# Kernel tuning notes

Measured on AMD Instinct MI355X. Metric: run time of the kernel, lower is better.

Reference implementation:

```python
import jax, jax.numpy as jnp
import numpy as np

M = 8      # number of modalities (len(ModalityType))
D = 256    # embedding_dim
B = 8192   # batch size


def setup_inputs() -> dict:
    key = jax.random.key(0)
    ks = jax.random.split(key, 12)
    s = 1.0 / np.sqrt(D)
    x = jax.random.normal(ks[0], (M, B, D), dtype=jnp.float32)
    reasoning_query = jax.random.normal(ks[1], (B, D), dtype=jnp.float32)
    # Per ordered modality pair (src, tgt): seq_len=1 MHA reduces to out_proj(V_proj(tgt)).
    Wv = jax.random.normal(ks[2], (M, M, D, D), dtype=jnp.float32) * s
    bv = jnp.zeros((M, M, D), dtype=jnp.float32)
    Wo = jax.random.normal(ks[3], (M, M, D, D), dtype=jnp.float32) * s
    bo = jnp.zeros((M, M, D), dtype=jnp.float32)
    # Per-modality fusion MLP: Linear(2D->D), ReLU, Linear(D->D)  (dropout = eval/identity)
    W1 = jax.random.normal(ks[4], (M, D, 2 * D), dtype=jnp.float32) * s
    b1 = jnp.zeros((M, D), dtype=jnp.float32)
    W2 = jax.random.normal(ks[5], (M, D, D), dtype=jnp.float32) * s
    b2 = jnp.zeros((M, D), dtype=jnp.float32)
    # Attention controller: Linear(2D->D), ReLU, Linear(D->1), Sigmoid
    Wc1 = jax.random.normal(ks[6], (D, 2 * D), dtype=jnp.float32) * s
    bc1 = jnp.zeros((D,), dtype=jnp.float32)
    wc2 = jax.random.normal(ks[7], (D,), dtype=jnp.float32) * s
    bc2 = jnp.zeros((1,), dtype=jnp.float32)
    return dict(x=x, reasoning_query=reasoning_query, Wv=Wv, bv=bv, Wo=Wo, bo=bo,
                W1=W1, b1=b1, W2=W2, b2=b2, Wc1=Wc1, bc1=bc1, wc2=wc2, bc2=bc2)


def reference(x, reasoning_query, Wv, bv, Wo, bo, W1, b1, W2, b2, Wc1, bc1, wc2, bc2):
    m = x.shape[0]
    # Cross-modal attention with seq_len=1: softmax over one key == 1, so the
    # attended output is exactly out_proj(V_proj(tgt_embedding)) for every pair.
    h = jnp.einsum('tbd,sted->stbe', x, Wv) + bv[:, :, None, :]          # [M,M,B,D]
    ctx = jnp.einsum('stbe,stoe->stbo', h, Wo) + bo[:, :, None, :]       # [M,M,B,D]
    # Mean over the M-1 target modalities (src != tgt), matching stack(...).mean(-1)
    offdiag = (1.0 - jnp.eye(m, dtype=x.dtype))[:, :, None, None]
    cross = (ctx * offdiag).sum(axis=1) / (m - 1)                         # [M,B,D]
    # Per-modality fusion MLP on cat([original, cross])
    comb = jnp.concatenate([x, cross], axis=-1)                           # [M,B,2D]
    hid = jax.nn.relu(jnp.einsum('mbf,mdf->mbd', comb, W1) + b1[:, None, :])
    fused = jnp.einsum('mbd,mod->mbo', hid, W2) + b2[:, None, :]          # [M,B,D]
    # Reasoning-query gating controller
    q = jnp.broadcast_to(reasoning_query[None], fused.shape)              # [M,B,D]
    qc = jnp.concatenate([q, fused], axis=-1)                             # [M,B,2D]
    ch = jax.nn.relu(jnp.einsum('mbf,df->mbd', qc, Wc1) + bc1)
    score = jax.nn.sigmoid(jnp.einsum('mbd,d->mb', ch, wc2) + bc2)        # [M,B]
    gated = fused * score[..., None]
    unified = gated.mean(axis=0)                                          # [B,D]
    return unified
```

## Files before the change

kernel.cpp:

```cpp
#include <hip/hip_runtime.h>

#define MMOD 8
#define BB 8192
#define DD 256

typedef unsigned short u16;
typedef __attribute__((ext_vector_type(8))) short s16x8;
typedef __attribute__((ext_vector_type(4))) float f32x4;
typedef __attribute__((ext_vector_type(8))) unsigned short u16x8;
typedef __attribute__((ext_vector_type(4))) unsigned short u16x4;
typedef __attribute__((ext_vector_type(4))) short s16x4;

typedef __attribute__((address_space(3))) unsigned short lds_u16;
typedef __attribute__((address_space(1))) const unsigned short gl_u16;

__device__ __forceinline__ float b2f(u16 u){ union{unsigned i; float f;} x; x.i=((unsigned)u)<<16; return x.f; }
__device__ __forceinline__ u16 f2b(float f){ union{float f; unsigned i;} x; x.f=f; unsigned r = x.i + 0x7FFF + ((x.i>>16)&1u); return (u16)(r>>16); }

__device__ __forceinline__ void async_cp16(const u16* g, u16* l){
  __builtin_amdgcn_global_load_lds((gl_u16*)g, (lds_u16*)l, 16, 0, 0);
}

struct ConvArgs {
  const float* src[10];
  u16*         dst[10];
  int          n[10];
  float*       cbz;
  const float* bc2;
  float*       bc2f;
};
__global__ void convert_kernel(ConvArgs a){
  const long long stride = (long long)gridDim.x * blockDim.x;
  const long long base   = (long long)blockIdx.x * blockDim.x + threadIdx.x;
  if (base < 2048) a.cbz[base] = 0.0f;
  if (base == 0)   a.bc2f[0] = a.bc2[0];
  for (int s = 0; s < 10; s++){
    const int n  = a.n[s];
    const int n8 = n >> 3;
    const float* sp = a.src[s];
    u16* dst = a.dst[s];
    for (long long i = base; i < n8; i += stride){
      float4 lo = ((const float4*)sp)[i*2];
      float4 hi = ((const float4*)sp)[i*2+1];
      u16x8 p;
      p[0]=f2b(lo.x); p[1]=f2b(lo.y); p[2]=f2b(lo.z); p[3]=f2b(lo.w);
      p[4]=f2b(hi.x); p[5]=f2b(hi.y); p[6]=f2b(hi.z); p[7]=f2b(hi.w);
      *(u16x8*)(dst + (i<<3)) = p;
    }
    for (long long i = ((long long)n8<<3) + base; i < n; i += stride)
      dst[i] = f2b(sp[i]);
  }
}

__device__ __forceinline__ s16x8 load8_f32(const float* p, long long idx){
  float4 lo = *(const float4*)(p + idx);
  float4 hi = *(const float4*)(p + idx + 4);
  s16x8 r;
  r[0]=(short)f2b(lo.x); r[1]=(short)f2b(lo.y); r[2]=(short)f2b(lo.z); r[3]=(short)f2b(lo.w);
  r[4]=(short)f2b(hi.x); r[5]=(short)f2b(hi.y); r[6]=(short)f2b(hi.z); r[7]=(short)f2b(hi.w);
  return r;
}

struct GArgs {
  const u16* A;  long long a_z; long long a_piece; int lda;
  const u16* A2; long long a2_z;
  const u16* B;  long long b_z; int ldb;
  u16*       C;  long long c_z; long long c_npiece; int ldc;
  const u16* bias; long long bias_z;
  const float* cbias;
  float scale;
  int K;
  int relu;
};

__global__ __launch_bounds__(512, 2) void gemm_8ph(GArgs g){
  alignas(16) __shared__ u16 L[65536];
  const int tid  = threadIdx.x;
  const int lane = tid & 63;
  const int w    = tid >> 6;

  const int wr  = w >> 2;
  const int wcn = w & 3;
  const int fm  = lane & 15;
  const int fq  = lane >> 4;

  const long long arow0 = (long long)blockIdx.x * 256;
  const long long nrow0 = (long long)blockIdx.y * 256;

  const int r0  = tid >> 3;
  const int r1  = r0 + 64;
  const int cs  = tid & 7;
  const int gc0 = cs ^ (r0 & 7);
  const int gc1 = cs ^ (r1 & 7);
  const int ldst0 = (w * 64) * 8;
  const int ldst1 = (512 + w * 64) * 8;

  const u16* Az = g.A;
  const u16* Bz = g.B;

  const long long gA0 = (arow0 + r0) * 256  + gc0 * 8;
  const long long gA1 = (arow0 + r1) * 256  + gc1 * 8;
  const long long gB0 = (nrow0 + r0) * 2048 + gc0 * 8;
  const long long gB1 = (nrow0 + r1) * 2048 + gc1 * 8;

#define STAGE_A8(c, k0s, h) do{ \
    const u16* gb_ = Az + (long long)((k0s) >> 8) * 2097152LL + ((k0s) & 255) + (long long)(h) * 32768LL; \
    u16* lb_ = L + ((c) * 2 + 0) * 16384 + (h) * 8192; \
    async_cp16(gb_ + gA0, lb_ + ldst0); \
    async_cp16(gb_ + gA1, lb_ + ldst1); \
  }while(0)
#define STAGE_B8(c, k0s, h) do{ \
    const u16* gb_ = Bz + (k0s) + (long long)(h) * 262144LL; \
    u16* lb_ = L + ((c) * 2 + 1) * 16384 + (h) * 8192; \
    async_cp16(gb_ + gB0, lb_ + ldst0); \
    async_cp16(gb_ + gB1, lb_ + ldst1); \
  }while(0)

  f32x4 acc[8][4];
  #pragma unroll
  for (int i=0;i<8;i++)
    #pragma unroll
    for (int j=0;j<4;j++)
      #pragma unroll
      for (int r=0;r<4;r++) acc[i][j][r] = 0.0f;

  const int T = g.K >> 6;

  STAGE_A8(0, 0, 0);  STAGE_A8(0, 0, 1);
  STAGE_B8(0, 0, 0);  STAGE_B8(0, 0, 1);
  STAGE_B8(1, 64, 0); STAGE_B8(1, 64, 1);
  asm volatile("s_waitcnt vmcnt(4)" ::: "memory");
  __builtin_amdgcn_s_barrier();

#define TILE8(cc, t) do{ \
    const int k0_ = (t) << 6; \
    const u16* lA_ = L + ((cc) * 2 + 0) * 16384; \
    const u16* lB_ = L + ((cc) * 2 + 1) * 16384; \
    s16x8 bf[4][2]; \
    _Pragma("unroll") \
    for (int q = 0; q < 4; ++q){ \
      if (q == 0 && (t) + 1 < T) STAGE_A8((cc) ^ 1, k0_ + 64, 0); \
      if (q == 1 && (t) + 1 < T) STAGE_A8((cc) ^ 1, k0_ + 64, 1); \
      if (q == 2 && (t) + 2 < T) STAGE_B8((cc),     k0_ + 128, 0); \
      if (q == 3 && (t) + 2 < T) STAGE_B8((cc),     k0_ + 128, 1); \
      if (q == 0){ \
        _Pragma("unroll") \
        for (int ni = 0; ni < 4; ni++){ \
          const int R = wcn * 64 + ni * 16 + fm; \
          _Pragma("unroll") \
          for (int kk = 0; kk < 2; kk++){ \
            const int qf = kk * 4 + fq; \
            bf[ni][kk] = *(const s16x8*)(lB_ + R * 64 + ((qf ^ (R & 7)) << 3)); \
          } \
        } \
      } \
      s16x8 af[2][2]; \
      _Pragma("unroll") \
      for (int j = 0; j < 2; j++){ \
        const int R = wr * 128 + (q * 2 + j) * 16 + fm; \
        _Pragma("unroll") \
        for (int kk = 0; kk < 2; kk++){ \
          const int qf = kk * 4 + fq; \
          af[j][kk] = *(const s16x8*)(lA_ + R * 64 + ((qf ^ (R & 7)) << 3)); \
        } \
      } \
      __builtin_amdgcn_s_barrier(); \
      __builtin_amdgcn_s_setprio(1); \
      _Pragma("unroll") \
      for (int kk = 0; kk < 2; kk++) \
        _Pragma("unroll") \
        for (int j = 0; j < 2; j++) \
          _Pragma("unroll") \
          for (int ni = 0; ni < 4; ni++) \
            acc[q*2+j][ni] = __builtin_amdgcn_mfma_f32_16x16x32_bf16(af[j][kk], bf[ni][kk], acc[q*2+j][ni], 0, 0, 0); \
      __builtin_amdgcn_s_setprio(0); \
      if (q == 3){ \
        if ((t) + 2 < T)      asm volatile("s_waitcnt vmcnt(4)" ::: "memory"); \
        else if ((t) + 1 < T) asm volatile("s_waitcnt vmcnt(0)" ::: "memory"); \
      } \
      __builtin_amdgcn_s_barrier(); \
    } \
  }while(0)

  for (int t = 0; t < T; t += 2){
    TILE8(0, t);
    TILE8(1, t + 1);
  }

  u16* Cb = g.C;
  #pragma unroll
  for (int mi = 0; mi < 8; mi++){
    #pragma unroll
    for (int ni = 0; ni < 4; ni++){
      const int n = (int)nrow0 + wcn * 64 + ni * 16 + fm;
      float bb = g.cbias ? g.cbias[n] : 0.0f;
      const long long cn = ((long long)(n >> 8)) * 2097152LL + (n & 255);
      #pragma unroll
      for (int r = 0; r < 4; r++){
        const long long b = arow0 + wr * 128 + mi * 16 + fq * 4 + r;
        float v = acc[mi][ni][r] * g.scale + bb;
        Cb[cn + b * 256] = f2b(v);
      }
    }
  }
#undef STAGE_A8
#undef STAGE_B8
#undef TILE8
}

__global__ __launch_bounds__(256, 4) void gemm_thin(GArgs g){
  alignas(16) __shared__ u16 lA[64*64];
  alignas(16) __shared__ u16 lB[256*64];
  const int tid  = threadIdx.x;
  const int lane = tid & 63;
  const int w    = tid >> 6;
  const int z    = blockIdx.z;

  const u16* Bbase = g.B + (long long)z * g.b_z;

  f32x4 acc[16];
  #pragma unroll
  for (int j=0;j<16;j++)
    #pragma unroll
    for (int r=0;r<4;r++) acc[j][r] = 0.0f;

  const int fm = lane & 15;
  const int fk = (lane >> 4) * 8;
  const long long arow0 = (long long)blockIdx.x * 64;

  const int sr = lane >> 3;
  const int sq = (lane & 7) ^ sr;

  for (int k0 = 0; k0 < g.K; k0 += 64){
    const u16* Abase0 = (g.A2 && k0 >= 256) ? (g.A2 + (long long)z * g.a2_z)
                                            : (g.A  + (long long)z * g.a_z);
    const u16* At = Abase0 + (long long)(k0 >> 8) * g.a_piece + (k0 & 255);
    const u16* Bt = Bbase + k0;
    __syncthreads();
    #pragma unroll
    for (int i=0;i<2;i++){
      int r = i*32 + w*8 + sr;
      async_cp16(At + (arow0 + r) * (long long)g.lda + sq*8, lA + (i*256 + w*64) * 8);
    }
    #pragma unroll
    for (int i=0;i<8;i++){
      int r = i*32 + w*8 + sr;
      async_cp16(Bt + (long long)r * g.ldb + sq*8, lB + (i*256 + w*64) * 8);
    }
    __syncthreads();
    #pragma unroll
    for (int kk = 0; kk < 64; kk += 32){
      const int qf = (kk + fk) >> 3;
      int ra = w*16 + fm;
      s16x8 af = *(const s16x8*)(lA + (ra*8 + (qf ^ (ra & 7))) * 8);
      #pragma unroll
      for (int ni=0; ni<16; ni++){
        int r = ni*16 + fm;
        s16x8 bfr = *(const s16x8*)(lB + (r*8 + (qf ^ (r & 7))) * 8);
        acc[ni] = __builtin_amdgcn_mfma_f32_16x16x32_bf16(af, bfr, acc[ni], 0, 0, 0);
      }
    }
  }

  u16* Cb = g.C + (long long)z * g.c_z;
  const u16* biasp = g.bias ? g.bias + (long long)z * g.bias_z : (const u16*)0;
  #pragma unroll
  for (int ni=0; ni<16; ni++){
    int n = ni*16 + fm;
    float bb = 0.0f;
    if (g.cbias) bb = g.cbias[n];
    else if (biasp) bb = b2f(biasp[n]);
    #pragma unroll
    for (int r=0; r<4; r++){
      long long b = arow0 + w*16 + (lane>>4)*4 + r;
      float v = acc[ni][r] * g.scale + bb;
      if (g.relu) v = v > 0.0f ? v : 0.0f;
      Cb[b * (long long)g.ldc + n] = f2b(v);
    }
  }
}

struct S34Args {
  const u16* X;
  const u16* CR;
  const u16* W1;
  const u16* W2;
  const u16* Wc1h;
  const u16* b1;
  const u16* b2;
  const u16* bc1;
  const u16* wc2;
  const u16* qctx;
  const float* bc2f;
  float*     scores;
  u16*       F;
};
__global__ __launch_bounds__(256, 2) void gemm_s345(S34Args a){
  alignas(16) __shared__ u16 lB[256*64];
  alignas(16) __shared__ u16 lH[64*256];
  u16* lA = lH;

  const int tid  = threadIdx.x;
  const int lane = tid & 63;
  const int w    = tid >> 6;
  const int z    = blockIdx.z;

  const int fm = lane & 15;
  const int fq = lane >> 4;
  const long long arow0 = (long long)blockIdx.x * 64;
  const long long BD = (long long)BB * DD;

  const int sr = lane >> 3;
  const int sq = (lane & 7) ^ sr;

  const u16* Xz  = a.X  + (long long)z * BD;
  const u16* CRz = a.CR + (long long)z * BD;
  const u16* W1z = a.W1 + (long long)z * 131072;
  const u16* W2z = a.W2 + (long long)z * 65536;

  f32x4 acc[16];
  #pragma unroll
  for (int j=0;j<16;j++)
    #pragma unroll
    for (int r=0;r<4;r++) acc[j][r] = 0.0f;

  for (int k0 = 0; k0 < 512; k0 += 64){
    const u16* At = (k0 < 256) ? (Xz + k0) : (CRz + (k0 - 256));
    const u16* Bt = W1z + k0;
    __syncthreads();
    #pragma unroll
    for (int i=0;i<2;i++){
      int r = i*32 + w*8 + sr;
      async_cp16(At + (arow0 + r) * 256 + sq*8, lA + (i*256 + w*64) * 8);
    }
    #pragma unroll
    for (int i=0;i<8;i++){
      int r = i*32 + w*8 + sr;
      async_cp16(Bt + (long long)r * 512 + sq*8, lB + (i*256 + w*64) * 8);
    }
    __syncthreads();
    #pragma unroll
    for (int kk = 0; kk < 64; kk += 32){
      const int qf = (kk >> 3) + fq;
      int ra = w*16 + fm;
      s16x8 af = *(const s16x8*)(lA + (ra*8 + (qf ^ (ra & 7))) * 8);
      #pragma unroll
      for (int ni=0; ni<16; ni++){
        int r = ni*16 + fm;
        s16x8 bfr = *(const s16x8*)(lB + (r*8 + (qf ^ (r & 7))) * 8);
        acc[ni] = __builtin_amdgcn_mfma_f32_16x16x32_bf16(bfr, af, acc[ni], 0, 0, 0);
      }
    }
  }

  __syncthreads();

  {
    const int b = w*16 + fm;
    #pragma unroll
    for (int ni=0; ni<16; ni++){
      s16x4 b1v = *(const s16x4*)(a.b1 + (long long)z*256 + ni*16 + fq*4);
      u16x4 pk;
      #pragma unroll
      for (int r=0; r<4; r++){
        float v = acc[ni][r] + b2f((u16)b1v[r]);
        v = v > 0.0f ? v : 0.0f;
        pk[r] = f2b(v);
      }
      const int c = ni*2 + (fq >> 1);
      const int csw = (c & ~7) | ((c & 7) ^ (b & 7));
      *(u16x4*)(lH + b*256 + csw*8 + (fq & 1)*4) = pk;
    }
  }

  f32x4 acc2[16];
  #pragma unroll
  for (int j=0;j<16;j++)
    #pragma unroll
    for (int r=0;r<4;r++) acc2[j][r] = 0.0f;

  for (int k0 = 0; k0 < 256; k0 += 64){
    const u16* Bt = W2z + k0;
    __syncthreads();
    #pragma unroll
    for (int i=0;i<8;i++){
      int r = i*32 + w*8 + sr;
      async_cp16(Bt + (long long)r * 256 + sq*8, lB + (i*256 + w*64) * 8);
    }
    __syncthreads();
    #pragma unroll
    for (int kk = 0; kk < 64; kk += 32){
      const int ra = w*16 + fm;
      const int qa = ((k0 + kk) >> 3) + fq;
      const int qsw = (qa & ~7) | ((qa & 7) ^ (ra & 7));
      s16x8 af = *(const s16x8*)(lH + ra*256 + qsw*8);
      const int qf = (kk >> 3) + fq;
      #pragma unroll
      for (int ni=0; ni<16; ni++){
        int r = ni*16 + fm;
        s16x8 bfr = *(const s16x8*)(lB + (r*8 + (qf ^ (r & 7))) * 8);
        acc2[ni] = __builtin_amdgcn_mfma_f32_16x16x32_bf16(bfr, af, acc2[ni], 0, 0, 0);
      }
    }
  }

  __syncthreads();

  {
    const int b = w*16 + fm;
    u16* Fz = a.F + (long long)z * BD;
    #pragma unroll
    for (int ni=0; ni<16; ni++){
      s16x4 b2v = *(const s16x4*)(a.b2 + (long long)z*256 + ni*16 + fq*4);
      u16x4 pk;
      #pragma unroll
      for (int r=0; r<4; r++)
        pk[r] = f2b(acc2[ni][r] + b2f((u16)b2v[r]));
      *(u16x4*)(Fz + (arow0 + b)*256 + ni*16 + fq*4) = pk;
      const int c = ni*2 + (fq >> 1);
      const int csw = (c & ~7) | ((c & 7) ^ (b & 7));
      *(u16x4*)(lH + b*256 + csw*8 + (fq & 1)*4) = pk;
    }
  }

  f32x4 acc3[16];
  #pragma unroll
  for (int j=0;j<16;j++)
    #pragma unroll
    for (int r=0;r<4;r++) acc3[j][r] = 0.0f;

  for (int k0 = 0; k0 < 256; k0 += 64){
    const u16* Bt = a.Wc1h + k0;
    __syncthreads();
    #pragma unroll
    for (int i=0;i<8;i++){
      int r = i*32 + w*8 + sr;
      async_cp16(Bt + (long long)r * 512 + sq*8, lB + (i*256 + w*64) * 8);
    }
    __syncthreads();
    #pragma unroll
    for (int kk = 0; kk < 64; kk += 32){
      const int ra = w*16 + fm;
      const int qa = ((k0 + kk) >> 3) + fq;
      const int qsw = (qa & ~7) | ((qa & 7) ^ (ra & 7));
      s16x8 af = *(const s16x8*)(lH + ra*256 + qsw*8);
      const int qf = (kk >> 3) + fq;
      #pragma unroll
      for (int ni=0; ni<16; ni++){
        int r = ni*16 + fm;
        s16x8 bfr = *(const s16x8*)(lB + (r*8 + (qf ^ (r & 7))) * 8);
        acc3[ni] = __builtin_amdgcn_mfma_f32_16x16x32_bf16(af, bfr, acc3[ni], 0, 0, 0);
      }
    }
  }

  float p[4] = {0.f, 0.f, 0.f, 0.f};
  #pragma unroll
  for (int ni=0; ni<16; ni++){
    int n = ni*16 + fm;
    float bb = b2f(a.bc1[n]);
    float wcv = b2f(a.wc2[n]);
    #pragma unroll
    for (int r=0; r<4; r++){
      long long b = arow0 + w*16 + fq*4 + r;
      float v = acc3[ni][r] + bb + b2f(a.qctx[b*256 + n]);
      v = v > 0.0f ? v : 0.0f;
      p[r] += v * wcv;
    }
  }
  #pragma unroll
  for (int r=0; r<4; r++){
    #pragma unroll
    for (int off=1; off<16; off<<=1) p[r] += __shfl_xor(p[r], off);
  }
  if (fm == 0){
    float bc2v = a.bc2f[0];
    #pragma unroll
    for (int r=0; r<4; r++){
      long long b = arow0 + w*16 + fq*4 + r;
      a.scores[(long long)z*BB + b] = 1.0f / (1.0f + __expf(-(p[r] + bc2v)));
    }
  }
}

__global__ __launch_bounds__(256, 2) void build_wb(const float* Wo, const float* Wv, u16* WB){
  alignas(16) __shared__ u16 lA[128*64];
  alignas(16) __shared__ u16 lB[128*64];
  const int tid  = threadIdx.x;
  const int lane = tid & 63;
  const int w    = tid >> 6;
  const int z = blockIdx.z, s = z >> 3, t = z & 7;
  const long long zoff = (long long)z * 65536;

  f32x4 acc[4][4];
  #pragma unroll
  for (int i=0;i<4;i++)
    #pragma unroll
    for (int j=0;j<4;j++)
      #pragma unroll
      for (int r=0;r<4;r++) acc[i][j][r] = 0.0f;

  const int wr = (w >> 1) * 64, wc = (w & 1) * 64;
  const int fm = lane & 15;
  const int fk = (lane >> 4) * 8;

  int srow[4], sq[4];
  #pragma unroll
  for (int i=0;i<4;i++){
    int c = i*256 + tid;
    srow[i] = c >> 3;
    sq[i]   = (c & 7) ^ (srow[i] & 7);
  }

  for (int k0 = 0; k0 < 256; k0 += 64){
    s16x8 va[4], vt[4];
    #pragma unroll
    for (int i=0;i<4;i++){
      long long aidx = zoff + (long long)(blockIdx.x*128 + srow[i]) * 256 + k0 + sq[i]*8;
      va[i] = load8_f32(Wo, aidx);
    }
    #pragma unroll
    for (int j=0;j<4;j++){
      int id = j*256 + tid;
      int e  = id >> 4;
      int dc = (id & 15) * 8;
      long long bidx = zoff + (long long)(k0 + e) * 256 + blockIdx.y*128 + dc;
      vt[j] = load8_f32(Wv, bidx);
    }
    __syncthreads();
    #pragma unroll
    for (int i=0;i<4;i++){
      int c = i*256 + tid;
      *(s16x8*)(lA + c*8) = va[i];
    }
    #pragma unroll
    for (int j=0;j<4;j++){
      int id = j*256 + tid;
      int e  = id >> 4;
      int dc = (id & 15) * 8;
      #pragma unroll
      for (int u=0; u<8; u++){
        int d = dc + u;
        lB[(d*8 + ((e>>3) ^ (d & 7)))*8 + (e & 7)] = (u16)vt[j][u];
      }
    }
    __syncthreads();
    #pragma unroll
    for (int kk = 0; kk < 64; kk += 32){
      s16x8 af[4], bfr[4];
      const int qf = (kk + fk) >> 3;
      #pragma unroll
      for (int mi=0; mi<4; mi++){
        int r = wr + mi*16 + fm;
        af[mi] = *(const s16x8*)(lA + (r*8 + (qf ^ (r & 7))) * 8);
      }
      #pragma unroll
      for (int ni=0; ni<4; ni++){
        int r = wc + ni*16 + fm;
        bfr[ni] = *(const s16x8*)(lB + (r*8 + (qf ^ (r & 7))) * 8);
      }
      #pragma unroll
      for (int mi=0; mi<4; mi++)
        #pragma unroll
        for (int ni=0; ni<4; ni++)
          acc[mi][ni] = __builtin_amdgcn_mfma_f32_16x16x32_bf16(af[mi], bfr[ni], acc[mi][ni], 0, 0, 0);
    }
    __syncthreads();
  }
  const int diag = (s == t);
  #pragma unroll
  for (int mi=0; mi<4; mi++){
    #pragma unroll
    for (int ni=0; ni<4; ni++){
      int d = blockIdx.y*128 + wc + ni*16 + fm;
      #pragma unroll
      for (int r=0; r<4; r++){
        int o = blockIdx.x*128 + wr + mi*16 + (lane>>4)*4 + r;
        float v = diag ? 0.0f : acc[mi][ni][r];
        WB[(long long)(s*256 + o) * 2048 + t*256 + d] = f2b(v);
      }
    }
  }
}

__global__ __launch_bounds__(256) void cb_kernel(const float* bv, const float* Wo, const float* bo, float* cb){
  int z = blockIdx.x, s = z >> 3, t = z & 7;
  if (s == t) return;
  int lane = threadIdx.x & 63, w = threadIdx.x >> 6;
  float4 bvv = *(const float4*)(bv + (long long)z*256 + lane*4);
  #pragma unroll
  for (int i=0; i<16; i++){
    int row = blockIdx.y*64 + w*16 + i;
    float4 wv4 = *(const float4*)(Wo + (long long)z*65536 + (long long)row*256 + lane*4);
    float p = wv4.x*bvv.x + wv4.y*bvv.y + wv4.z*bvv.z + wv4.w*bvv.w;
    #pragma unroll
    for (int off=32; off>0; off>>=1) p += __shfl_xor(p, off);
    if (lane == 0)
      atomicAdd(&cb[s*256 + row], (p + bo[(long long)z*256 + row]) * (1.0f/7.0f));
  }
}

__global__ __launch_bounds__(256) void final_gate(const u16* fused, const float* scores, float* out){
  int b = blockIdx.x;
  int tid = threadIdx.x;
  float sc[8];
  #pragma unroll
  for (int m=0; m<8; m++) sc[m] = scores[(long long)m*BB + b];
  float acc = 0.0f;
  #pragma unroll
  for (int m=0; m<8; m++)
    acc += b2f(fused[((long long)m*BB + b)*256 + tid]) * sc[m];
  out[(long long)b*256 + tid] = acc * 0.125f;
}

extern "C" void kernel_launch(void* const* d_in, const int* in_sizes, int n_in,
                              void* d_out, int out_size, void* d_ws, size_t ws_size,
                              hipStream_t stream){
  const float* x   = (const float*)d_in[0];
  const float* q   = (const float*)d_in[1];
  const float* Wv  = (const float*)d_in[2];
  const float* bv  = (const float*)d_in[3];
  const float* Wo  = (const float*)d_in[4];
  const float* bo  = (const float*)d_in[5];
  const float* W1  = (const float*)d_in[6];
  const float* b1  = (const float*)d_in[7];
  const float* W2  = (const float*)d_in[8];
  const float* b2  = (const float*)d_in[9];
  const float* Wc1 = (const float*)d_in[10];
  const float* bc1 = (const float*)d_in[11];
  const float* wc2 = (const float*)d_in[12];
  const float* bc2 = (const float*)d_in[13];

  char* ws = (char*)d_ws;
  u16*   xb    = (u16*)(ws + 0LL);
  u16*   qb    = (u16*)(ws + 33554432LL);
  u16*   cross = (u16*)(ws + 37748736LL);
  u16*   WB    = (u16*)(ws + 104857600LL);
  u16*   W1b   = (u16*)(ws + 113246208LL);
  u16*   W2b   = (u16*)(ws + 115343360LL);
  u16*   Wc1b  = (u16*)(ws + 116391936LL);
  u16*   b1b   = (u16*)(ws + 116654080LL);
  u16*   b2b   = (u16*)(ws + 116658176LL);
  u16*   bc1b  = (u16*)(ws + 116662272LL);
  u16*   wc2b  = (u16*)(ws + 116662784LL);
  float* bc2f  = (float*)(ws + 116663296LL);
  float* cb    = (float*)(ws + 116663424LL);
  u16*   fused = xb;
  u16*   qctx  = WB;
  float* scores = (float*)(ws + 104857600LL + 4194304LL);

  ConvArgs ca{};
  ca.src[0]=x;   ca.dst[0]=xb;   ca.n[0]=MMOD*BB*DD;
  ca.src[1]=q;   ca.dst[1]=qb;   ca.n[1]=BB*DD;
  ca.src[2]=W1;  ca.dst[2]=W1b;  ca.n[2]=MMOD*DD*2*DD;
  ca.src[3]=W2;  ca.dst[3]=W2b;  ca.n[3]=MMOD*DD*DD;
  ca.src[4]=Wc1; ca.dst[4]=Wc1b; ca.n[4]=DD*2*DD;
  ca.src[5]=b1;  ca.dst[5]=b1b;  ca.n[5]=MMOD*DD;
  ca.src[6]=b2;  ca.dst[6]=b2b;  ca.n[6]=MMOD*DD;
  ca.src[7]=bc1; ca.dst[7]=bc1b; ca.n[7]=DD;
  ca.src[8]=wc2; ca.dst[8]=wc2b; ca.n[8]=DD;
  ca.src[9]=bc2; ca.dst[9]=bc1b; ca.n[9]=0;
  ca.cbz = cb; ca.bc2 = bc2; ca.bc2f = bc2f;
  convert_kernel<<<1024, 256, 0, stream>>>(ca);

  build_wb<<<dim3(2,2,64), 256, 0, stream>>>(Wo, Wv, WB);
  cb_kernel<<<dim3(64,4), 256, 0, stream>>>(bv, Wo, bo, cb);

  const long long BD = (long long)BB * DD;

  GArgs g2{};
  g2.A = xb; g2.a_z = 0; g2.a_piece = BD; g2.lda = 256; g2.A2 = 0; g2.a2_z = 0;
  g2.B = WB; g2.b_z = 0; g2.ldb = 2048;
  g2.C = cross; g2.c_z = 0; g2.c_npiece = BD; g2.ldc = 256;
  g2.bias = 0; g2.bias_z = 0; g2.cbias = cb;
  g2.scale = 1.0f/7.0f; g2.K = 2048; g2.relu = 0;
  gemm_8ph<<<dim3(32,8,1), 512, 0, stream>>>(g2);

  GArgs g5a{};
  g5a.A = qb; g5a.a_z = 0; g5a.a_piece = 0; g5a.lda = 256; g5a.A2 = 0; g5a.a2_z = 0;
  g5a.B = Wc1b; g5a.b_z = 0; g5a.ldb = 512;
  g5a.C = qctx; g5a.c_z = 0; g5a.c_npiece = 0; g5a.ldc = 256;
  g5a.bias = 0; g5a.bias_z = 0; g5a.cbias = 0;
  g5a.scale = 1.0f; g5a.K = 256; g5a.relu = 0;
  gemm_thin<<<dim3(128,1,1), 256, 0, stream>>>(g5a);

  S34Args s34{};
  s34.X = xb; s34.CR = cross; s34.W1 = W1b; s34.W2 = W2b; s34.Wc1h = Wc1b + 256;
  s34.b1 = b1b; s34.b2 = b2b; s34.bc1 = bc1b; s34.wc2 = wc2b;
  s34.qctx = qctx; s34.bc2f = bc2f; s34.scores = scores; s34.F = fused;
  gemm_s345<<<dim3(128,1,8), 256, 0, stream>>>(s34);

  final_gate<<<dim3(BB), 256, 0, stream>>>(fused, scores, (float*)d_out);

  (void)in_sizes; (void)n_in; (void)out_size; (void)ws_size;
}
```

Before: 328.1 us.

## Merge prep kernels and skip diagonal K-blocks in cross GEMM

The fp32-to-bf16 conversion, the WB weight-product build and the combined-bias computation now run as one prep kernel whose blocks branch by index, removing two launches and the atomic bias accumulation. The cross GEMM skips the four K tiles of the diagonal (src==tgt) block, which were zero, by remapping K indices, so it iterates over 28 tiles instead of 32. WB diagonal blocks are no longer written, which is safe only because they are never read. final_gate now uses a grid-stride loop over 1024 blocks.

After: 316.8 us. 1.04x faster.

```diff
diff --git a/kernel.cpp b/kernel.cpp
--- a/kernel.cpp
+++ b/kernel.cpp
@@ -19,37 +19,6 @@
 
 __device__ __forceinline__ void async_cp16(const u16* g, u16* l){
   __builtin_amdgcn_global_load_lds((gl_u16*)g, (lds_u16*)l, 16, 0, 0);
-}
-
-struct ConvArgs {
-  const float* src[10];
-  u16*         dst[10];
-  int          n[10];
-  float*       cbz;
-  const float* bc2;
-  float*       bc2f;
-};
-__global__ void convert_kernel(ConvArgs a){
-  const long long stride = (long long)gridDim.x * blockDim.x;
-  const long long base   = (long long)blockIdx.x * blockDim.x + threadIdx.x;
-  if (base < 2048) a.cbz[base] = 0.0f;
-  if (base == 0)   a.bc2f[0] = a.bc2[0];
-  for (int s = 0; s < 10; s++){
-    const int n  = a.n[s];
-    const int n8 = n >> 3;
-    const float* sp = a.src[s];
-    u16* dst = a.dst[s];
-    for (long long i = base; i < n8; i += stride){
-      float4 lo = ((const float4*)sp)[i*2];
-      float4 hi = ((const float4*)sp)[i*2+1];
-      u16x8 p;
-      p[0]=f2b(lo.x); p[1]=f2b(lo.y); p[2]=f2b(lo.z); p[3]=f2b(lo.w);
-      p[4]=f2b(hi.x); p[5]=f2b(hi.y); p[6]=f2b(hi.z); p[7]=f2b(hi.w);
-      *(u16x8*)(dst + (i<<3)) = p;
-    }
-    for (long long i = ((long long)n8<<3) + base; i < n; i += stride)
-      dst[i] = f2b(sp[i]);
-  }
 }
 
 __device__ __forceinline__ s16x8 load8_f32(const float* p, long long idx){
@@ -59,6 +28,181 @@
   r[0]=(short)f2b(lo.x); r[1]=(short)f2b(lo.y); r[2]=(short)f2b(lo.z); r[3]=(short)f2b(lo.w);
   r[4]=(short)f2b(hi.x); r[5]=(short)f2b(hi.y); r[6]=(short)f2b(hi.z); r[7]=(short)f2b(hi.w);
   return r;
+}
+
+struct PrepArgs {
+  const float* src[10];
+  u16*         dst[10];
+  int          n[10];
+  const float* bc2;
+  float*       bc2f;
+  const float* Wo;
+  const float* Wv;
+  u16*         WB;
+  const float* bv;
+  const float* bo;
+  float*       cb;
+};
+__global__ __launch_bounds__(256, 3) void prep_kernel(PrepArgs a){
+  alignas(16) __shared__ u16 lA[128*64];
+  alignas(16) __shared__ u16 lB[128*64];
+  const int tid = threadIdx.x;
+  const unsigned bxg = blockIdx.x;
+
+  if (bxg < 1024){
+    const long long stride = 1024LL * 256LL;
+    const long long base   = (long long)bxg * 256 + tid;
+    if (base == 0) a.bc2f[0] = a.bc2[0];
+    for (int s = 0; s < 10; s++){
+      const int n  = a.n[s];
+      const int n8 = n >> 3;
+      const float* sp = a.src[s];
+      u16* dst = a.dst[s];
+      for (long long i = base; i < n8; i += stride){
+        float4 lo = ((const float4*)sp)[i*2];
+        float4 hi = ((const float4*)sp)[i*2+1];
+        u16x8 p;
+        p[0]=f2b(lo.x); p[1]=f2b(lo.y); p[2]=f2b(lo.z); p[3]=f2b(lo.w);
+        p[4]=f2b(hi.x); p[5]=f2b(hi.y); p[6]=f2b(hi.z); p[7]=f2b(hi.w);
+        *(u16x8*)(dst + (i<<3)) = p;
+      }
+      for (long long i = ((long long)n8<<3) + base; i < n; i += stride)
+        dst[i] = f2b(sp[i]);
+    }
+  } else if (bxg < 1280){
+    const int f  = (int)bxg - 1024;
+    const int bwx = f & 1, bwy = (f >> 1) & 1, z = f >> 2;
+    const int s = z >> 3, t = z & 7;
+    if (s == t) return;
+    const long long zoff = (long long)z * 65536;
+    const int lane = tid & 63;
+    const int w    = tid >> 6;
+
+    f32x4 acc[4][4];
+    #pragma unroll
+    for (int i=0;i<4;i++)
+      #pragma unroll
+      for (int j=0;j<4;j++)
+        #pragma unroll
+        for (int r=0;r<4;r++) acc[i][j][r] = 0.0f;
+
+    const int wr = (w >> 1) * 64, wc = (w & 1) * 64;
+    const int fm = lane & 15;
+    const int fk = (lane >> 4) * 8;
+
+    int srow[4], sq[4];
+    #pragma unroll
+    for (int i=0;i<4;i++){
+      int c = i*256 + tid;
+      srow[i] = c >> 3;
+      sq[i]   = (c & 7) ^ (srow[i] & 7);
+    }
+
+    for (int k0 = 0; k0 < 256; k0 += 64){
+      s16x8 va[4], vt[4];
+      #pragma unroll
+      for (int i=0;i<4;i++){
+        long long aidx = zoff + (long long)(bwx*128 + srow[i]) * 256 + k0 + sq[i]*8;
+        va[i] = load8_f32(a.Wo, aidx);
+      }
+      #pragma unroll
+      for (int j=0;j<4;j++){
+        int id = j*256 + tid;
+        int e  = id >> 4;
+        int dc = (id & 15) * 8;
+        long long bidx = zoff + (long long)(k0 + e) * 256 + bwy*128 + dc;
+        vt[j] = load8_f32(a.Wv, bidx);
+      }
+      __syncthreads();
+      #pragma unroll
+      for (int i=0;i<4;i++){
+        int c = i*256 + tid;
+        *(s16x8*)(lA + c*8) = va[i];
+      }
+      #pragma unroll
+      for (int j=0;j<4;j++){
+        int id = j*256 + tid;
+        int e  = id >> 4;
+        int dc = (id & 15) * 8;
+        #pragma unroll
+        for (int u=0; u<8; u++){
+          int d = dc + u;
+          lB[(d*8 + ((e>>3) ^ (d & 7)))*8 + (e & 7)] = (u16)vt[j][u];
+        }
+      }
+      __syncthreads();
+      #pragma unroll
+      for (int kk = 0; kk < 64; kk += 32){
+        s16x8 af[4], bfr[4];
+        const int qf = (kk + fk) >> 3;
+        #pragma unroll
+        for (int mi=0; mi<4; mi++){
+          int r = wr + mi*16 + fm;
+          af[mi] = *(const s16x8*)(lA + (r*8 + (qf ^ (r & 7))) * 8);
+        }
+        #pragma unroll
+        for (int ni=0; ni<4; ni++){
+          int r = wc + ni*16 + fm;
+          bfr[ni] = *(const s16x8*)(lB + (r*8 + (qf ^ (r & 7))) * 8);
+        }
+        #pragma unroll
+        for (int mi=0; mi<4; mi++)
+          #pragma unroll
+          for (int ni=0; ni<4; ni++)
+            acc[mi][ni] = __builtin_amdgcn_mfma_f32_16x16x32_bf16(af[mi], bfr[ni], acc[mi][ni], 0, 0, 0);
+      }
+      __syncthreads();
+    }
+    #pragma unroll
+    for (int mi=0; mi<4; mi++){
+      #pragma unroll
+      for (int ni=0; ni<4; ni++){
+        int d = bwy*128 + wc + ni*16 + fm;
+        #pragma unroll
+        for (int r=0; r<4; r++){
+          int o = bwx*128 + wr + mi*16 + (lane>>4)*4 + r;
+          a.WB[(long long)(s*256 + o) * 2048 + t*256 + d] = f2b(acc[mi][ni][r]);
+        }
+      }
+    }
+  } else {
+    const int f = (int)bxg - 1280;
+    const int s = f >> 2, chunk = f & 3;
+    const int lane = tid & 63, wv = tid >> 6;
+    float pp[16];
+    #pragma unroll
+    for (int i=0;i<16;i++) pp[i] = 0.0f;
+    #pragma unroll
+    for (int t2 = 0; t2 < 8; t2++){
+      if (t2 == s) continue;
+      const int z = s*8 + t2;
+      float4 bvv = *(const float4*)(a.bv + (long long)z*256 + lane*4);
+      #pragma unroll
+      for (int i=0;i<16;i++){
+        int row = chunk*64 + wv*16 + i;
+        float4 w4 = *(const float4*)(a.Wo + (long long)z*65536 + (long long)row*256 + lane*4);
+        pp[i] += w4.x*bvv.x + w4.y*bvv.y + w4.z*bvv.z + w4.w*bvv.w;
+      }
+    }
+    #pragma unroll
+    for (int i=0;i<16;i++){
+      #pragma unroll
+      for (int off=32; off>0; off>>=1) pp[i] += __shfl_xor(pp[i], off);
+    }
+    if (lane == 0){
+      #pragma unroll
+      for (int i=0;i<16;i++){
+        int row = chunk*64 + wv*16 + i;
+        float bos = 0.0f;
+        #pragma unroll
+        for (int t2=0; t2<8; t2++){
+          if (t2 == s) continue;
+          bos += a.bo[(long long)(s*8+t2)*256 + row];
+        }
+        a.cb[s*256 + row] = (pp[i] + bos) * (1.0f/7.0f);
+      }
+    }
+  }
 }
 
 struct GArgs {
@@ -86,6 +230,7 @@
 
   const long long arow0 = (long long)blockIdx.x * 256;
   const long long nrow0 = (long long)blockIdx.y * 256;
+  const int ny4 = (int)blockIdx.y * 4;
 
   const int r0  = tid >> 3;
   const int r1  = r0 + 64;
@@ -102,6 +247,8 @@
   const long long gA1 = (arow0 + r1) * 256  + gc1 * 8;
   const long long gB0 = (nrow0 + r0) * 2048 + gc0 * 8;
   const long long gB1 = (nrow0 + r1) * 2048 + gc1 * 8;
+
+#define MAPK(j) ((((j) >= ny4) ? (j) + 4 : (j)) << 6)
 
 #define STAGE_A8(c, k0s, h) do{ \
     const u16* gb_ = Az + (long long)((k0s) >> 8) * 2097152LL + ((k0s) & 255) + (long long)(h) * 32768LL; \
@@ -124,25 +271,22 @@
       #pragma unroll
       for (int r=0;r<4;r++) acc[i][j][r] = 0.0f;
 
-  const int T = g.K >> 6;
-
-  STAGE_A8(0, 0, 0);  STAGE_A8(0, 0, 1);
-  STAGE_B8(0, 0, 0);  STAGE_B8(0, 0, 1);
-  STAGE_B8(1, 64, 0); STAGE_B8(1, 64, 1);
+  STAGE_A8(0, MAPK(0), 0);  STAGE_A8(0, MAPK(0), 1);
+  STAGE_B8(0, MAPK(0), 0);  STAGE_B8(0, MAPK(0), 1);
+  STAGE_B8(1, MAPK(1), 0);  STAGE_B8(1, MAPK(1), 1);
   asm volatile("s_waitcnt vmcnt(4)" ::: "memory");
   __builtin_amdgcn_s_barrier();
 
-#define TILE8(cc, t) do{ \
-    const int k0_ = (t) << 6; \
+#define TILE8(cc, k0n1, k0n2, v1, v2) do{ \
     const u16* lA_ = L + ((cc) * 2 + 0) * 16384; \
     const u16* lB_ = L + ((cc) * 2 + 1) * 16384; \
     s16x8 bf[4][2]; \
     _Pragma("unroll") \
     for (int q = 0; q < 4; ++q){ \
-      if (q == 0 && (t) + 1 < T) STAGE_A8((cc) ^ 1, k0_ + 64, 0); \
-      if (q == 1 && (t) + 1 < T) STAGE_A8((cc) ^ 1, k0_ + 64, 1); \
-      if (q == 2 && (t) + 2 < T) STAGE_B8((cc),     k0_ + 128, 0); \
-      if (q == 3 && (t) + 2 < T) STAGE_B8((cc),     k0_ + 128, 1); \
+      if (q == 0 && (v1)) STAGE_A8((cc) ^ 1, (k0n1), 0); \
+      if (q == 1 && (v1)) STAGE_A8((cc) ^ 1, (k0n1), 1); \
+      if (q == 2 && (v2)) STAGE_B8((cc), (k0n2), 0); \
+      if (q == 3 && (v2)) STAGE_B8((cc), (k0n2), 1); \
       if (q == 0){ \
         _Pragma("unroll") \
         for (int ni = 0; ni < 4; ni++){ \
@@ -175,16 +319,17 @@
             acc[q*2+j][ni] = __builtin_amdgcn_mfma_f32_16x16x32_bf16(af[j][kk], bf[ni][kk], acc[q*2+j][ni], 0, 0, 0); \
       __builtin_amdgcn_s_setprio(0); \
       if (q == 3){ \
-        if ((t) + 2 < T)      asm volatile("s_waitcnt vmcnt(4)" ::: "memory"); \
-        else if ((t) + 1 < T) asm volatile("s_waitcnt vmcnt(0)" ::: "memory"); \
+        if (v2)      asm volatile("s_waitcnt vmcnt(4)" ::: "memory"); \
+        else if (v1) asm volatile("s_waitcnt vmcnt(0)" ::: "memory"); \
       } \
       __builtin_amdgcn_s_barrier(); \
     } \
   }while(0)
 
-  for (int t = 0; t < T; t += 2){
-    TILE8(0, t);
-    TILE8(1, t + 1);
+  #pragma unroll 1
+  for (int j = 0; j < 28; j += 2){
+    TILE8(0, MAPK(j+1), MAPK(j+2), (j+1) < 28, (j+2) < 28);
+    TILE8(1, MAPK(j+2), MAPK(j+3), (j+2) < 28, (j+3) < 28);
   }
 
   u16* Cb = g.C;
@@ -206,6 +351,7 @@
 #undef STAGE_A8
 #undef STAGE_B8
 #undef TILE8
+#undef MAPK
 }
 
 __global__ __launch_bounds__(256, 4) void gemm_thin(GArgs g){
@@ -483,134 +629,15 @@
   }
 }
 
-__global__ __launch_bounds__(256, 2) void build_wb(const float* Wo, const float* Wv, u16* WB){
-  alignas(16) __shared__ u16 lA[128*64];
-  alignas(16) __shared__ u16 lB[128*64];
-  const int tid  = threadIdx.x;
-  const int lane = tid & 63;
-  const int w    = tid >> 6;
-  const int z = blockIdx.z, s = z >> 3, t = z & 7;
-  const long long zoff = (long long)z * 65536;
-
-  f32x4 acc[4][4];
-  #pragma unroll
-  for (int i=0;i<4;i++)
-    #pragma unroll
-    for (int j=0;j<4;j++)
-      #pragma unroll
-      for (int r=0;r<4;r++) acc[i][j][r] = 0.0f;
-
-  const int wr = (w >> 1) * 64, wc = (w & 1) * 64;
-  const int fm = lane & 15;
-  const int fk = (lane >> 4) * 8;
-
-  int srow[4], sq[4];
-  #pragma unroll
-  for (int i=0;i<4;i++){
-    int c = i*256 + tid;
-    srow[i] = c >> 3;
-    sq[i]   = (c & 7) ^ (srow[i] & 7);
-  }
-
-  for (int k0 = 0; k0 < 256; k0 += 64){
-    s16x8 va[4], vt[4];
-    #pragma unroll
-    for (int i=0;i<4;i++){
-      long long aidx = zoff + (long long)(blockIdx.x*128 + srow[i]) * 256 + k0 + sq[i]*8;
-      va[i] = load8_f32(Wo, aidx);
-    }
-    #pragma unroll
-    for (int j=0;j<4;j++){
-      int id = j*256 + tid;
-      int e  = id >> 4;
-      int dc = (id & 15) * 8;
-      long long bidx = zoff + (long long)(k0 + e) * 256 + blockIdx.y*128 + dc;
-      vt[j] = load8_f32(Wv, bidx);
-    }
-    __syncthreads();
-    #pragma unroll
-    for (int i=0;i<4;i++){
-      int c = i*256 + tid;
-      *(s16x8*)(lA + c*8) = va[i];
-    }
-    #pragma unroll
-    for (int j=0;j<4;j++){
-      int id = j*256 + tid;
-      int e  = id >> 4;
-      int dc = (id & 15) * 8;
-      #pragma unroll
-      for (int u=0; u<8; u++){
-        int d = dc + u;
-        lB[(d*8 + ((e>>3) ^ (d & 7)))*8 + (e & 7)] = (u16)vt[j][u];
-      }
-    }
-    __syncthreads();
-    #pragma unroll
-    for (int kk = 0; kk < 64; kk += 32){
-      s16x8 af[4], bfr[4];
-      const int qf = (kk + fk) >> 3;
-      #pragma unroll
-      for (int mi=0; mi<4; mi++){
-        int r = wr + mi*16 + fm;
-        af[mi] = *(const s16x8*)(lA + (r*8 + (qf ^ (r & 7))) * 8);
-      }
-      #pragma unroll
-      for (int ni=0; ni<4; ni++){
-        int r = wc + ni*16 + fm;
-        bfr[ni] = *(const s16x8*)(lB + (r*8 + (qf ^ (r & 7))) * 8);
-      }
-      #pragma unroll
-      for (int mi=0; mi<4; mi++)
-        #pragma unroll
-        for (int ni=0; ni<4; ni++)
-          acc[mi][ni] = __builtin_amdgcn_mfma_f32_16x16x32_bf16(af[mi], bfr[ni], acc[mi][ni], 0, 0, 0);
-    }
-    __syncthreads();
-  }
-  const int diag = (s == t);
-  #pragma unroll
-  for (int mi=0; mi<4; mi++){
-    #pragma unroll
-    for (int ni=0; ni<4; ni++){
-      int d = blockIdx.y*128 + wc + ni*16 + fm;
-      #pragma unroll
-      for (int r=0; r<4; r++){
-        int o = blockIdx.x*128 + wr + mi*16 + (lane>>4)*4 + r;
-        float v = diag ? 0.0f : acc[mi][ni][r];
-        WB[(long long)(s*256 + o) * 2048 + t*256 + d] = f2b(v);
-      }
-    }
-  }
-}
-
-__global__ __launch_bounds__(256) void cb_kernel(const float* bv, const float* Wo, const float* bo, float* cb){
-  int z = blockIdx.x, s = z >> 3, t = z & 7;
-  if (s == t) return;
-  int lane = threadIdx.x & 63, w = threadIdx.x >> 6;
-  float4 bvv = *(const float4*)(bv + (long long)z*256 + lane*4);
-  #pragma unroll
-  for (int i=0; i<16; i++){
-    int row = blockIdx.y*64 + w*16 + i;
-    float4 wv4 = *(const float4*)(Wo + (long long)z*65536 + (long long)row*256 + lane*4);
-    float p = wv4.x*bvv.x + wv4.y*bvv.y + wv4.z*bvv.z + wv4.w*bvv.w;
-    #pragma unroll
-    for (int off=32; off>0; off>>=1) p += __shfl_xor(p, off);
-    if (lane == 0)
-      atomicAdd(&cb[s*256 + row], (p + bo[(long long)z*256 + row]) * (1.0f/7.0f));
-  }
-}
-
 __global__ __launch_bounds__(256) void final_gate(const u16* fused, const float* scores, float* out){
-  int b = blockIdx.x;
-  int tid = threadIdx.x;
-  float sc[8];
-  #pragma unroll
-  for (int m=0; m<8; m++) sc[m] = scores[(long long)m*BB + b];
-  float acc = 0.0f;
-  #pragma unroll
-  for (int m=0; m<8; m++)
-    acc += b2f(fused[((long long)m*BB + b)*256 + tid]) * sc[m];
-  out[(long long)b*256 + tid] = acc * 0.125f;
+  const int tid = threadIdx.x;
+  for (int b = blockIdx.x; b < BB; b += gridDim.x){
+    float acc = 0.0f;
+    #pragma unroll
+    for (int m=0; m<8; m++)
+      acc += b2f(fused[((long long)m*BB + b)*256 + tid]) * scores[(long long)m*BB + b];
+    out[(long long)b*256 + tid] = acc * 0.125f;
+  }
 }
 
 extern "C" void kernel_launch(void* const* d_in, const int* in_sizes, int n_in,
@@ -649,22 +676,21 @@
   u16*   qctx  = WB;
   float* scores = (float*)(ws + 104857600LL + 4194304LL);
 
-  ConvArgs ca{};
-  ca.src[0]=x;   ca.dst[0]=xb;   ca.n[0]=MMOD*BB*DD;
-  ca.src[1]=q;   ca.dst[1]=qb;   ca.n[1]=BB*DD;
-  ca.src[2]=W1;  ca.dst[2]=W1b;  ca.n[2]=MMOD*DD*2*DD;
-  ca.src[3]=W2;  ca.dst[3]=W2b;  ca.n[3]=MMOD*DD*DD;
-  ca.src[4]=Wc1; ca.dst[4]=Wc1b; ca.n[4]=DD*2*DD;
-  ca.src[5]=b1;  ca.dst[5]=b1b;  ca.n[5]=MMOD*DD;
-  ca.src[6]=b2;  ca.dst[6]=b2b;  ca.n[6]=MMOD*DD;
-  ca.src[7]=bc1; ca.dst[7]=bc1b; ca.n[7]=DD;
-  ca.src[8]=wc2; ca.dst[8]=wc2b; ca.n[8]=DD;
-  ca.src[9]=bc2; ca.dst[9]=bc1b; ca.n[9]=0;
-  ca.cbz = cb; ca.bc2 = bc2; ca.bc2f = bc2f;
-  convert_kernel<<<1024, 256, 0, stream>>>(ca);
-
-  build_wb<<<dim3(2,2,64), 256, 0, stream>>>(Wo, Wv, WB);
-  cb_kernel<<<dim3(64,4), 256, 0, stream>>>(bv, Wo, bo, cb);
+  PrepArgs pa{};
+  pa.src[0]=x;   pa.dst[0]=xb;   pa.n[0]=MMOD*BB*DD;
+  pa.src[1]=q;   pa.dst[1]=qb;   pa.n[1]=BB*DD;
+  pa.src[2]=W1;  pa.dst[2]=W1b;  pa.n[2]=MMOD*DD*2*DD;
+  pa.src[3]=W2;  pa.dst[3]=W2b;  pa.n[3]=MMOD*DD*DD;
+  pa.src[4]=Wc1; pa.dst[4]=Wc1b; pa.n[4]=DD*2*DD;
+  pa.src[5]=b1;  pa.dst[5]=b1b;  pa.n[5]=MMOD*DD;
+  pa.src[6]=b2;  pa.dst[6]=b2b;  pa.n[6]=MMOD*DD;
+  pa.src[7]=bc1; pa.dst[7]=bc1b; pa.n[7]=DD;
+  pa.src[8]=wc2; pa.dst[8]=wc2b; pa.n[8]=DD;
+  pa.src[9]=bc2; pa.dst[9]=bc1b; pa.n[9]=0;
+  pa.bc2 = bc2; pa.bc2f = bc2f;
+  pa.Wo = Wo; pa.Wv = Wv; pa.WB = WB;
+  pa.bv = bv; pa.bo = bo; pa.cb = cb;
+  prep_kernel<<<1312, 256, 0, stream>>>(pa);
 
   const long long BD = (long long)BB * DD;
 
@@ -690,7 +716,7 @@
   s34.qctx = qctx; s34.bc2f = bc2f; s34.scores = scores; s34.F = fused;
   gemm_s345<<<dim3(128,1,8), 256, 0, stream>>>(s34);
 
-  final_gate<<<dim3(BB), 256, 0, stream>>>(fused, scores, (float*)d_out);
+  final_gate<<<dim3(1024), 256, 0, stream>>>(fused, scores, (float*)d_out);
 
   (void)in_sizes; (void)n_in; (void)out_size; (void)ws_size;
 }
```
